# Kernel tuning notes

Hardware: AMD Instinct MI355X
Metric: run time of the kernel (lower is better)

Reference implementation:

```python
import jax, jax.numpy as jnp
import numpy as np

TOP_K = 2  # config.top_k


def setup_inputs() -> dict:
    key = jax.random.key(0)
    k0, k1, k2, k3, k4 = jax.random.split(key, 5)
    B, S, D, F, E = 1, 2048, 512, 1024, 8
    scale = 0.02
    hidden_states = jax.random.normal(k0, (B, S, D), dtype=jnp.float32)
    router_w = jax.random.normal(k1, (D, E), dtype=jnp.float32) * scale
    w1 = jax.random.normal(k2, (E, D, F), dtype=jnp.float32) * scale  # gate proj
    w2 = jax.random.normal(k3, (E, F, D), dtype=jnp.float32) * scale  # down proj
    w3 = jax.random.normal(k4, (E, D, F), dtype=jnp.float32) * scale  # up proj
    return {"hidden_states": hidden_states, "router_w": router_w,
            "w1": w1, "w2": w2, "w3": w3}


def reference(hidden_states, router_w, w1, w2, w3):
    B, S, D = hidden_states.shape
    E = router_w.shape[1]
    x = hidden_states.reshape(-1, D)                      # [T, D]
    T = x.shape[0]

    # router: softmax in float32, top-k, renormalize (matches torch source)
    router_logits = x @ router_w                          # [T, E]
    probs = jax.nn.softmax(router_logits.astype(jnp.float32), axis=-1)
    routing_weights, selected_experts = jax.lax.top_k(probs, TOP_K)  # [T, K]
    routing_weights = routing_weights / routing_weights.sum(axis=-1, keepdims=True)
    routing_weights = routing_weights.astype(x.dtype)

    # combine weights: scatter top-k weights into dense [T, E] (one-hot combine)
    combine = jnp.zeros((T, E), dtype=x.dtype).at[
        jnp.arange(T)[:, None], selected_experts].add(routing_weights)

    # dense-all-experts evaluation, math-identical to gather-GEMM-scatter:
    # unselected experts get combine weight 0 and contribute nothing.
    gate = jax.nn.silu(jnp.einsum('td,edf->tef', x, w1))  # [T, E, F]
    up = jnp.einsum('td,edf->tef', x, w3)                 # [T, E, F]
    h = gate * up * combine[:, :, None]                   # weight before down-proj
    out = jnp.einsum('tef,efd->td', h, w2)                # [T, D]
    return out.reshape(B, S, D)
```

## Files before the change

kernel.cpp:

```cpp
#include <hip/hip_runtime.h>
#include <hip/hip_bf16.h>


typedef __attribute__((ext_vector_type(4))) float f32x4;
typedef __attribute__((ext_vector_type(8))) __bf16 bf16x8;

#define T_TOK 2048
#define DMODEL 512
#define FFN 1024
#define NE 8
#define MAXMB 40
#define PCAP (MAXMB * 128)

__device__ __forceinline__ void gload_lds16(const void* g, void* l) {
  __builtin_amdgcn_global_load_lds(
      (const __attribute__((address_space(1))) void*)g,
      (__attribute__((address_space(3))) void*)l, 16, 0, 0);
}

#define PIPE_BAR_8()                                        \
  asm volatile("s_waitcnt vmcnt(8)" ::: "memory");          \
  __builtin_amdgcn_s_barrier();                             \
  __builtin_amdgcn_sched_barrier(0)
#define PIPE_BAR_6()                                        \
  asm volatile("s_waitcnt vmcnt(6)" ::: "memory");          \
  __builtin_amdgcn_s_barrier();                             \
  __builtin_amdgcn_sched_barrier(0)
#define PIPE_BAR_0()                                        \
  asm volatile("s_waitcnt vmcnt(0)" ::: "memory");          \
  __builtin_amdgcn_s_barrier();                             \
  __builtin_amdgcn_sched_barrier(0)
#define POST_BAR()                                          \
  __builtin_amdgcn_s_barrier();                             \
  __builtin_amdgcn_sched_barrier(0)

__global__ __launch_bounds__(256) void cvt_router_kernel(
    const float* __restrict__ x, const float* __restrict__ rw,
    __bf16* __restrict__ xb, int* __restrict__ tope, float* __restrict__ topw) {
  const int t = blockIdx.x * 4 + (threadIdx.x >> 6);
  const int lane = threadIdx.x & 63;
  const float* xr = x + (size_t)t * DMODEL + lane * 8;
  const f32x4 a = *(const f32x4*)xr;
  const f32x4 b = *(const f32x4*)(xr + 4);
  bf16x8 v;
  v[0] = (__bf16)a[0]; v[1] = (__bf16)a[1]; v[2] = (__bf16)a[2]; v[3] = (__bf16)a[3];
  v[4] = (__bf16)b[0]; v[5] = (__bf16)b[1]; v[6] = (__bf16)b[2]; v[7] = (__bf16)b[3];
  *(bf16x8*)&xb[(size_t)t * DMODEL + lane * 8] = v;

  float xv[8] = {a[0], a[1], a[2], a[3], b[0], b[1], b[2], b[3]};
  float part[NE];
#pragma unroll
  for (int e = 0; e < NE; ++e) part[e] = 0.f;
#pragma unroll
  for (int i = 0; i < 8; ++i) {
    const int d = lane * 8 + i;
    const f32x4 r0 = *(const f32x4*)&rw[(size_t)d * NE];
    const f32x4 r1 = *(const f32x4*)&rw[(size_t)d * NE + 4];
    part[0] += xv[i] * r0[0]; part[1] += xv[i] * r0[1];
    part[2] += xv[i] * r0[2]; part[3] += xv[i] * r0[3];
    part[4] += xv[i] * r1[0]; part[5] += xv[i] * r1[1];
    part[6] += xv[i] * r1[2]; part[7] += xv[i] * r1[3];
  }
#pragma unroll
  for (int off = 32; off > 0; off >>= 1) {
#pragma unroll
    for (int e = 0; e < NE; ++e) part[e] += __shfl_xor(part[e], off);
  }
  if (lane == 0) {
    int ia = 0;
#pragma unroll
    for (int e = 1; e < NE; ++e)
      if (part[e] > part[ia]) ia = e;
    int ib = (ia == 0) ? 1 : 0;
#pragma unroll
    for (int e = 0; e < NE; ++e)
      if (e != ia && e != ib && part[e] > part[ib]) ib = e;
    const float wa = 1.f / (1.f + __expf(part[ib] - part[ia]));
    tope[t * 2] = ia;
    tope[t * 2 + 1] = ib;
    topw[t * 2] = wa;
    topw[t * 2 + 1] = 1.f - wa;
  }
}

__global__ __launch_bounds__(256) void build_kernel(
    const int* __restrict__ tope, const float* __restrict__ topw,
    int* __restrict__ pair_t, float* __restrict__ pair_w,
    int* __restrict__ pairidx, int* __restrict__ sched_e) {
  __shared__ int cnt[NE], base[NE], ofs[NE];
  const int tid = threadIdx.x;
  if (tid < NE) { cnt[tid] = 0; ofs[tid] = 0; }
  for (int i = tid; i < PCAP; i += 256) { pair_t[i] = 0; pair_w[i] = 0.f; }
  for (int i = tid; i < MAXMB; i += 256) sched_e[i] = -1;
  __syncthreads();
  for (int t = tid; t < T_TOK; t += 256) {
    atomicAdd(&cnt[tope[t * 2]], 1);
    atomicAdd(&cnt[tope[t * 2 + 1]], 1);
  }
  __syncthreads();
  if (tid == 0) {
    int mb = 0;
    for (int e = 0; e < NE; ++e) {
      base[e] = mb * 128;
      const int nmb = (cnt[e] + 127) >> 7;
      for (int i = 0; i < nmb; ++i) sched_e[mb + i] = e;
      mb += nmb;
    }
  }
  __syncthreads();
  for (int t = tid; t < T_TOK; t += 256) {
#pragma unroll
    for (int s = 0; s < 2; ++s) {
      const int e = tope[t * 2 + s];
      const int pos = base[e] + atomicAdd(&ofs[e], 1);
      pair_t[pos] = t;
      pair_w[pos] = topw[t * 2 + s];
      pairidx[t * 2 + s] = pos;
    }
  }
}

__global__ __launch_bounds__(256) void transpose_all_kernel(
    const float* __restrict__ w1, const float* __restrict__ w2,
    const float* __restrict__ w3, __bf16* __restrict__ w1t,
    __bf16* __restrict__ w2t, __bf16* __restrict__ w3t) {
  __shared__ __bf16 tile[64][65];
  const int tid = threadIdx.x;
  const int bx = blockIdx.x;
  const float* src;
  __bf16* dst;
  int R, C, idx;
  if (bx < 1024)      { src = w1; dst = w1t; R = 512;  C = 1024; idx = bx; }
  else if (bx < 2048) { src = w3; dst = w3t; R = 512;  C = 1024; idx = bx - 1024; }
  else                { src = w2; dst = w2t; R = 1024; C = 512;  idx = bx - 2048; }
  const int ntx = C >> 6, nty = R >> 6;
  const int cx = idx % ntx;
  const int gry = idx / ntx;
  const int e = gry / nty;
  const int r0 = (gry % nty) * 64;
  const int c0 = cx * 64;
  src += (size_t)e * R * C;
  dst += (size_t)e * R * C;
#pragma unroll
  for (int q = 0; q < 4; ++q) {
    const int r = (tid >> 4) + q * 16;
    const int c = (tid & 15) * 4;
    const f32x4 v = *(const f32x4*)&src[(size_t)(r0 + r) * C + c0 + c];
    tile[r][c] = (__bf16)v[0];
    tile[r][c + 1] = (__bf16)v[1];
    tile[r][c + 2] = (__bf16)v[2];
    tile[r][c + 3] = (__bf16)v[3];
  }
  __syncthreads();
#pragma unroll
  for (int p = 0; p < 2; ++p) {
    const int cc = (tid >> 3) + p * 32;
    const int rr = (tid & 7) * 8;
    union { bf16x8 v; __bf16 s[8]; } u;
#pragma unroll
    for (int i = 0; i < 8; ++i) u.s[i] = tile[rr + i][cc];
    *(bf16x8*)&dst[(size_t)(c0 + cc) * R + r0 + rr] = u.v;
  }
}

__global__ __launch_bounds__(256) void gemm1_kernel(
    const __bf16* __restrict__ xb, const __bf16* __restrict__ w1t,
    const __bf16* __restrict__ w3t, const int* __restrict__ pair_t,
    const float* __restrict__ pair_w, const int* __restrict__ sched_e,
    __bf16* __restrict__ hbuf) {
  __shared__ alignas(16) __bf16 As[2][128 * 64];
  __shared__ alignas(16) __bf16 B1s[2][64 * 64];
  __shared__ alignas(16) __bf16 B3s[2][64 * 64];
  __shared__ float comb[128];
  const int tid = threadIdx.x;
  const int mb = blockIdx.y;
  const int e = sched_e[mb];
  if (e < 0) return;
  const int m0 = mb * 128;
  const int f0 = blockIdx.x * 64;
  const int lane = tid & 63;
  const int wv = tid >> 6;
  const int wr = wv >> 1, wc = wv & 1;
  const int l15 = lane & 15, lhi = lane >> 4;
  const int sw = (l15 & 7) << 4;

  if (tid < 128) comb[tid] = pair_w[m0 + tid];

  size_t aoff[4];
  int lbA[4];
#pragma unroll
  for (int it = 0; it < 4; ++it) {
    const int chunk = it * 256 + tid;
    const int r = chunk >> 3;
    const int c8 = ((chunk & 7) ^ (r & 7)) * 8;
    aoff[it] = (size_t)pair_t[m0 + r] * DMODEL + c8;
    lbA[it] = (it * 256 + (tid & ~63)) * 16;
  }
  size_t boff[2];
  int lbB[2];
#pragma unroll
  for (int it = 0; it < 2; ++it) {
    const int chunk = it * 256 + tid;
    const int r = chunk >> 3;
    const int c8 = ((chunk & 7) ^ (r & 7)) * 8;
    boff[it] = (size_t)(e * FFN + f0 + r) * DMODEL + c8;
    lbB[it] = (it * 256 + (tid & ~63)) * 16;
  }

  const f32x4 fz = {0.f, 0.f, 0.f, 0.f};
  f32x4 acc1[4][2], acc3[4][2];
#pragma unroll
  for (int m = 0; m < 4; ++m)
#pragma unroll
    for (int n = 0; n < 2; ++n) { acc1[m][n] = fz; acc3[m][n] = fz; }

#define G1_STAGE(BUF, K0)                                                     \
  do {                                                                        \
    _Pragma("unroll") for (int it = 0; it < 4; ++it)                          \
        gload_lds16(xb + aoff[it] + (K0), (char*)As[BUF] + lbA[it]);          \
    _Pragma("unroll") for (int it = 0; it < 2; ++it) {                        \
      gload_lds16(w1t + boff[it] + (K0), (char*)B1s[BUF] + lbB[it]);          \
      gload_lds16(w3t + boff[it] + (K0), (char*)B3s[BUF] + lbB[it]);          \
    }                                                                         \
  } while (0)

#define G1_COMPUTE(BUF)                                                       \
  do {                                                                        \
    __builtin_amdgcn_s_setprio(1);                                            \
    _Pragma("unroll") for (int kk = 0; kk < 2; ++kk) {                        \
      const int ko = (kk * 64 + lhi * 16) ^ sw;                               \
      bf16x8 af[4], b1f[2], b3f[2];                                           \
      _Pragma("unroll") for (int m = 0; m < 4; ++m)                           \
          af[m] = *(const bf16x8*)((const char*)As[BUF] +                     \
                                   (wr * 64 + m * 16 + l15) * 128 + ko);      \
      _Pragma("unroll") for (int n = 0; n < 2; ++n) {                         \
        const int ro = (wc * 32 + n * 16 + l15) * 128 + ko;                   \
        b1f[n] = *(const bf16x8*)((const char*)B1s[BUF] + ro);                \
        b3f[n] = *(const bf16x8*)((const char*)B3s[BUF] + ro);                \
      }                                                                       \
      _Pragma("unroll") for (int m = 0; m < 4; ++m)                           \
          _Pragma("unroll") for (int n = 0; n < 2; ++n) {                     \
        acc1[m][n] = __builtin_amdgcn_mfma_f32_16x16x32_bf16(af[m], b1f[n],   \
                                                             acc1[m][n], 0, 0, 0); \
        acc3[m][n] = __builtin_amdgcn_mfma_f32_16x16x32_bf16(af[m], b3f[n],   \
                                                             acc3[m][n], 0, 0, 0); \
      }                                                                       \
    }                                                                         \
    __builtin_amdgcn_s_setprio(0);                                            \
  } while (0)

  G1_STAGE(0, 0);
#pragma unroll
  for (int t = 0; t < 7; ++t) {
    G1_STAGE((t + 1) & 1, (t + 1) * 64);
    PIPE_BAR_8();
    G1_COMPUTE(t & 1);
    POST_BAR();
  }
  PIPE_BAR_0();
  G1_COMPUTE(1);

#pragma unroll
  for (int m = 0; m < 4; ++m)
#pragma unroll
    for (int n = 0; n < 2; ++n)
#pragma unroll
      for (int r = 0; r < 4; ++r) {
        const int row = wr * 64 + m * 16 + lhi * 4 + r;
        const int col = wc * 32 + n * 16 + l15;
        const float g = acc1[m][n][r];
        const float u = acc3[m][n][r];
        const float val = (g / (1.f + __expf(-g))) * u * comb[row];
        hbuf[(size_t)(m0 + row) * FFN + f0 + col] = (__bf16)val;
      }
#undef G1_STAGE
#undef G1_COMPUTE
}

__global__ __launch_bounds__(256) void gemm2_kernel(
    const __bf16* __restrict__ hbuf, const __bf16* __restrict__ w2t,
    const int* __restrict__ sched_e, float* __restrict__ outp) {
  __shared__ alignas(16) __bf16 As[2][128 * 64];
  __shared__ alignas(16) __bf16 Bs[2][64 * 64];
  const int tid = threadIdx.x;
  const int mb = blockIdx.y;
  const int e = sched_e[mb];
  if (e < 0) return;
  const int m0 = mb * 128;
  const int n0 = blockIdx.x * 64;
  const int kz = blockIdx.z;
  const int fbase = kz * (FFN / 2);
  const int lane = tid & 63;
  const int wv = tid >> 6;
  const int wr = wv >> 1, wc = wv & 1;
  const int l15 = lane & 15, lhi = lane >> 4;
  const int sw = (l15 & 7) << 4;

  size_t aoff[4];
  int lbA[4];
#pragma unroll
  for (int it = 0; it < 4; ++it) {
    const int chunk = it * 256 + tid;
    const int r = chunk >> 3;
    const int c8 = ((chunk & 7) ^ (r & 7)) * 8;
    aoff[it] = (size_t)(m0 + r) * FFN + fbase + c8;
    lbA[it] = (it * 256 + (tid & ~63)) * 16;
  }
  size_t boff[2];
  int lbB[2];
#pragma unroll
  for (int it = 0; it < 2; ++it) {
    const int chunk = it * 256 + tid;
    const int r = chunk >> 3;
    const int c8 = ((chunk & 7) ^ (r & 7)) * 8;
    boff[it] = ((size_t)e * DMODEL + n0 + r) * FFN + fbase + c8;
    lbB[it] = (it * 256 + (tid & ~63)) * 16;
  }

  const f32x4 fz = {0.f, 0.f, 0.f, 0.f};
  f32x4 acc[4][2];
#pragma unroll
  for (int m = 0; m < 4; ++m) { acc[m][0] = fz; acc[m][1] = fz; }

#define G2_STAGE(BUF, K0)                                                     \
  do {                                                                        \
    _Pragma("unroll") for (int it = 0; it < 4; ++it)                          \
        gload_lds16(hbuf + aoff[it] + (K0), (char*)As[BUF] + lbA[it]);        \
    _Pragma("unroll") for (int it = 0; it < 2; ++it)                          \
        gload_lds16(w2t + boff[it] + (K0), (char*)Bs[BUF] + lbB[it]);         \
  } while (0)

#define G2_COMPUTE(BUF)                                                       \
  do {                                                                        \
    __builtin_amdgcn_s_setprio(1);                                            \
    _Pragma("unroll") for (int kk = 0; kk < 2; ++kk) {                        \
      const int ko = (kk * 64 + lhi * 16) ^ sw;                               \
      bf16x8 af[4], bfr[2];                                                   \
      _Pragma("unroll") for (int m = 0; m < 4; ++m)                           \
          af[m] = *(const bf16x8*)((const char*)As[BUF] +                     \
                                   (wr * 64 + m * 16 + l15) * 128 + ko);      \
      _Pragma("unroll") for (int n = 0; n < 2; ++n)                           \
          bfr[n] = *(const bf16x8*)((const char*)Bs[BUF] +                    \
                                    (wc * 32 + n * 16 + l15) * 128 + ko);     \
      _Pragma("unroll") for (int m = 0; m < 4; ++m)                           \
          _Pragma("unroll") for (int n = 0; n < 2; ++n)                       \
              acc[m][n] = __builtin_amdgcn_mfma_f32_16x16x32_bf16(            \
                  af[m], bfr[n], acc[m][n], 0, 0, 0);                         \
    }                                                                         \
    __builtin_amdgcn_s_setprio(0);                                            \
  } while (0)

  G2_STAGE(0, 0);
#pragma unroll
  for (int t = 0; t < 7; ++t) {
    G2_STAGE((t + 1) & 1, (t + 1) * 64);
    PIPE_BAR_6();
    G2_COMPUTE(t & 1);
    POST_BAR();
  }
  PIPE_BAR_0();
  G2_COMPUTE(1);

#pragma unroll
  for (int m = 0; m < 4; ++m)
#pragma unroll
    for (int n = 0; n < 2; ++n)
#pragma unroll
      for (int r = 0; r < 4; ++r) {
        const int row = wr * 64 + m * 16 + lhi * 4 + r;
        const int col = wc * 32 + n * 16 + l15;
        outp[((size_t)kz * PCAP + m0 + row) * DMODEL + n0 + col] = acc[m][n][r];
      }
#undef G2_STAGE
#undef G2_COMPUTE
}

__global__ __launch_bounds__(256) void gather_kernel(
    const float* __restrict__ outp, const int* __restrict__ pairidx,
    float* __restrict__ out) {
  const int i = blockIdx.x * 256 + threadIdx.x;
  const int t = i >> 7;
  const int c = i & 127;
  const int p0 = pairidx[t * 2];
  const int p1 = pairidx[t * 2 + 1];
  const f32x4* O = (const f32x4*)outp;
  const size_t KZ = (size_t)PCAP * (DMODEL / 4);
  const size_t s0 = (size_t)p0 * (DMODEL / 4) + c;
  const size_t s1 = (size_t)p1 * (DMODEL / 4) + c;
  f32x4 v = O[s0] + O[s1] + O[s0 + KZ] + O[s1 + KZ];
  ((f32x4*)out)[i] = v;
}

extern "C" void kernel_launch(void* const* d_in, const int* in_sizes, int n_in,
                              void* d_out, int out_size, void* d_ws, size_t ws_size,
                              hipStream_t stream) {
  const float* x = (const float*)d_in[0];
  const float* rw = (const float*)d_in[1];
  const float* w1 = (const float*)d_in[2];
  const float* w2 = (const float*)d_in[3];
  const float* w3 = (const float*)d_in[4];
  float* out = (float*)d_out;
  char* ws = (char*)d_ws;

  int* tope = (int*)(ws + 0);
  float* topw = (float*)(ws + 16384);
  int* pair_t = (int*)(ws + 32768);
  float* pair_w = (float*)(ws + 53248);
  int* pairidx = (int*)(ws + 73728);
  int* sched_e = (int*)(ws + 90112);
  __bf16* xb = (__bf16*)(ws + 98304);
  __bf16* w1t = (__bf16*)(ws + 2195456);
  __bf16* w3t = (__bf16*)(ws + 10584064);
  __bf16* w2t = (__bf16*)(ws + 18972672);
  __bf16* hbuf = (__bf16*)(ws + 27361280);
  float* outp = (float*)(ws + 37847040);

  hipLaunchKernelGGL(cvt_router_kernel, dim3(T_TOK / 4), dim3(256), 0, stream, x, rw, xb, tope, topw);
  hipLaunchKernelGGL(build_kernel, dim3(1), dim3(256), 0, stream, tope, topw, pair_t, pair_w, pairidx, sched_e);
  hipLaunchKernelGGL(transpose_all_kernel, dim3(3072), dim3(256), 0, stream, w1, w2, w3, w1t, w2t, w3t);
  hipLaunchKernelGGL(gemm1_kernel, dim3(16, MAXMB), dim3(256), 0, stream, xb, w1t, w3t, pair_t, pair_w, sched_e, hbuf);
  hipLaunchKernelGGL(gemm2_kernel, dim3(8, MAXMB, 2), dim3(256), 0, stream, hbuf, w2t, sched_e, outp);
  hipLaunchKernelGGL(gather_kernel, dim3(1024), dim3(256), 0, stream, outp, pairidx, out);
}
```

Measured before the change: 78.11 us.

## Remap GEMM block indices for XCD locality and store split-K partials in bf16

Both GEMM kernels now use a flattened 1D grid with a custom block-to-tile mapping. Groups of 8 consecutive block IDs take different M blocks, or different (M, K-split) pairs, so blocks that share the same weight tiles likely land on different XCDs in a chosen pattern aimed at better L2 reuse. The split-K partial outputs of gemm2 are stored as bf16 instead of fp32, which halves the write and gather-read traffic. The gather kernel reads 8 bf16 values per thread and accumulates in fp32. The cost is extra rounding error from truncating the partial sums to bf16.

```diff
diff --git a/kernel.cpp b/kernel.cpp
--- a/kernel.cpp
+++ b/kernel.cpp
@@ -173,11 +173,12 @@
   __shared__ alignas(16) __bf16 B3s[2][64 * 64];
   __shared__ float comb[128];
   const int tid = threadIdx.x;
-  const int mb = blockIdx.y;
+  const int id = blockIdx.x;
+  const int mb = (id & 7) + ((id >> 7) << 3);
+  const int f0 = ((id >> 3) & 15) * 64;
   const int e = sched_e[mb];
   if (e < 0) return;
   const int m0 = mb * 128;
-  const int f0 = blockIdx.x * 64;
   const int lane = tid & 63;
   const int wv = tid >> 6;
   const int wr = wv >> 1, wc = wv & 1;
@@ -279,16 +280,18 @@
 
 __global__ __launch_bounds__(256) void gemm2_kernel(
     const __bf16* __restrict__ hbuf, const __bf16* __restrict__ w2t,
-    const int* __restrict__ sched_e, float* __restrict__ outp) {
+    const int* __restrict__ sched_e, __bf16* __restrict__ outp) {
   __shared__ alignas(16) __bf16 As[2][128 * 64];
   __shared__ alignas(16) __bf16 Bs[2][64 * 64];
   const int tid = threadIdx.x;
-  const int mb = blockIdx.y;
+  const int id = blockIdx.x;
+  const int gk = (id & 7) + ((id >> 6) << 3);
+  const int n0 = ((id >> 3) & 7) * 64;
+  const int mb = gk >> 1;
+  const int kz = gk & 1;
   const int e = sched_e[mb];
   if (e < 0) return;
   const int m0 = mb * 128;
-  const int n0 = blockIdx.x * 64;
-  const int kz = blockIdx.z;
   const int fbase = kz * (FFN / 2);
   const int lane = tid & 63;
   const int wv = tid >> 6;
@@ -369,26 +372,36 @@
       for (int r = 0; r < 4; ++r) {
         const int row = wr * 64 + m * 16 + lhi * 4 + r;
         const int col = wc * 32 + n * 16 + l15;
-        outp[((size_t)kz * PCAP + m0 + row) * DMODEL + n0 + col] = acc[m][n][r];
+        outp[((size_t)kz * PCAP + m0 + row) * DMODEL + n0 + col] =
+            (__bf16)acc[m][n][r];
       }
 #undef G2_STAGE
 #undef G2_COMPUTE
 }
 
 __global__ __launch_bounds__(256) void gather_kernel(
-    const float* __restrict__ outp, const int* __restrict__ pairidx,
+    const __bf16* __restrict__ outp, const int* __restrict__ pairidx,
     float* __restrict__ out) {
   const int i = blockIdx.x * 256 + threadIdx.x;
-  const int t = i >> 7;
-  const int c = i & 127;
+  const int t = i >> 6;
+  const int c = (i & 63) * 8;
   const int p0 = pairidx[t * 2];
   const int p1 = pairidx[t * 2 + 1];
-  const f32x4* O = (const f32x4*)outp;
-  const size_t KZ = (size_t)PCAP * (DMODEL / 4);
-  const size_t s0 = (size_t)p0 * (DMODEL / 4) + c;
-  const size_t s1 = (size_t)p1 * (DMODEL / 4) + c;
-  f32x4 v = O[s0] + O[s1] + O[s0 + KZ] + O[s1 + KZ];
-  ((f32x4*)out)[i] = v;
+  const size_t KZ = (size_t)PCAP * DMODEL;
+  const bf16x8 a0 = *(const bf16x8*)&outp[(size_t)p0 * DMODEL + c];
+  const bf16x8 a1 = *(const bf16x8*)&outp[(size_t)p1 * DMODEL + c];
+  const bf16x8 b0 = *(const bf16x8*)&outp[KZ + (size_t)p0 * DMODEL + c];
+  const bf16x8 b1 = *(const bf16x8*)&outp[KZ + (size_t)p1 * DMODEL + c];
+  f32x4 lo, hi;
+#pragma unroll
+  for (int j = 0; j < 4; ++j)
+    lo[j] = (float)a0[j] + (float)a1[j] + (float)b0[j] + (float)b1[j];
+#pragma unroll
+  for (int j = 0; j < 4; ++j)
+    hi[j] = (float)a0[j + 4] + (float)a1[j + 4] + (float)b0[j + 4] + (float)b1[j + 4];
+  float* op = out + (size_t)t * DMODEL + c;
+  *(f32x4*)op = lo;
+  *(f32x4*)(op + 4) = hi;
 }
 
 extern "C" void kernel_launch(void* const* d_in, const int* in_sizes, int n_in,
@@ -413,12 +426,12 @@
   __bf16* w3t = (__bf16*)(ws + 10584064);
   __bf16* w2t = (__bf16*)(ws + 18972672);
   __bf16* hbuf = (__bf16*)(ws + 27361280);
-  float* outp = (float*)(ws + 37847040);
+  __bf16* outp = (__bf16*)(ws + 37847040);
 
   hipLaunchKernelGGL(cvt_router_kernel, dim3(T_TOK / 4), dim3(256), 0, stream, x, rw, xb, tope, topw);
   hipLaunchKernelGGL(build_kernel, dim3(1), dim3(256), 0, stream, tope, topw, pair_t, pair_w, pairidx, sched_e);
   hipLaunchKernelGGL(transpose_all_kernel, dim3(3072), dim3(256), 0, stream, w1, w2, w3, w1t, w2t, w3t);
-  hipLaunchKernelGGL(gemm1_kernel, dim3(16, MAXMB), dim3(256), 0, stream, xb, w1t, w3t, pair_t, pair_w, sched_e, hbuf);
-  hipLaunchKernelGGL(gemm2_kernel, dim3(8, MAXMB, 2), dim3(256), 0, stream, hbuf, w2t, sched_e, outp);
-  hipLaunchKernelGGL(gather_kernel, dim3(1024), dim3(256), 0, stream, outp, pairidx, out);
-}
+  hipLaunchKernelGGL(gemm1_kernel, dim3(640), dim3(256), 0, stream, xb, w1t, w3t, pair_t, pair_w, sched_e, hbuf);
+  hipLaunchKernelGGL(gemm2_kernel, dim3(640), dim3(256), 0, stream, hbuf, w2t, sched_e, outp);
+  hipLaunchKernelGGL(gather_kernel, dim3(512), dim3(256), 0, stream, outp, pairidx, out);
+}
```

Measured after the change: 74.09 us. 1.05x faster.
